# Kernel optimization log

Measured on AMD Instinct MI355X. Metric: run time of the kernel, lower is better.

The kernel has to match this reference:

```python
import jax, jax.numpy as jnp
import numpy as np

D_MODEL = 768
N_HEADS = 8
HEAD_DIM = D_MODEL // N_HEADS
LN_EPS = 1e-5

def setup_inputs() -> dict:
    key = jax.random.key(0)
    k1, k2, k3 = jax.random.split(key, 3)
    B, L = 8, 4096
    x = jax.random.normal(k1, (B, L, D_MODEL), dtype=jnp.float32)
    gamma = jnp.ones((D_MODEL,), dtype=jnp.float32)
    beta = jnp.zeros((D_MODEL,), dtype=jnp.float32)
    # torch Linear weights transposed so forward is x @ W
    w_qkv = jax.random.normal(k2, (D_MODEL, 3 * D_MODEL), dtype=jnp.float32) * (1.0 / np.sqrt(D_MODEL))
    w_out = jax.random.normal(k3, (D_MODEL, D_MODEL), dtype=jnp.float32) * (1.0 / np.sqrt(D_MODEL))
    return {"x": x, "gamma": gamma, "beta": beta, "w_qkv": w_qkv, "w_out": w_out}

def reference(x, gamma, beta, w_qkv, w_out):
    B, L, D = x.shape
    residual = x
    # LayerNorm
    mu = jnp.mean(x, axis=-1, keepdims=True)
    var = jnp.mean(jnp.square(x - mu), axis=-1, keepdims=True)
    xn = (x - mu) * jax.lax.rsqrt(var + LN_EPS) * gamma + beta
    # qkv projection, split, reshape to [B, H, L, d]
    qkv = xn @ w_qkv  # [B, L, 3D]
    q, k, v = jnp.split(qkv, 3, axis=-1)
    def to_heads(t):
        return t.reshape(B, L, N_HEADS, HEAD_DIM).transpose(0, 2, 1, 3)
    q, k, v = to_heads(q), to_heads(k), to_heads(v)
    # feature maps: elu + 1
    q = jax.nn.elu(q) + 1.0
    k = jax.nn.elu(k) + 1.0
    # linear attention: kv aggregation then query readout
    kv = jnp.einsum('bhld,bhlv->bhdv', k, v)          # [B,H,d,d]
    out = jnp.einsum('bhld,bhdv->bhlv', q, kv)         # [B,H,L,d]
    k_sum = jnp.sum(k, axis=2)                         # [B,H,d]
    normalizer = jnp.einsum('bhld,bhd->bhl', q, k_sum) # [B,H,L]
    normalizer = jnp.maximum(normalizer, 1e-6)
    out = out / normalizer[..., None]
    out = out.transpose(0, 2, 1, 3).reshape(B, L, D)
    out = out @ w_out
    return out + residual
```

## Files before the change

### kernel.cpp

```cpp
#include <hip/hip_runtime.h>
#include <stdint.h>

#define D_MODEL 768
#define N3      2304
#define NHEAD   8
#define DH      96
#define BATCH   8
#define SEQ     4096
#define ROWS    (BATCH*SEQ)
#define LN_EPS  1e-5f

typedef __attribute__((ext_vector_type(8))) __bf16 bf16x8;
typedef __attribute__((ext_vector_type(4))) float f32x4;
typedef __attribute__((ext_vector_type(8))) unsigned short ushort8;
typedef __attribute__((ext_vector_type(4))) unsigned short ushort4v;

__device__ __forceinline__ unsigned short f2bf(float f) {
  union { float f; unsigned int u; } v; v.f = f;
  unsigned int r = v.u + 0x7FFFu + ((v.u >> 16) & 1u);
  return (unsigned short)(r >> 16);
}
__device__ __forceinline__ float bf2f(unsigned short u) {
  union { unsigned int u; float f; } v; v.u = ((unsigned int)u) << 16;
  return v.f;
}

#define GLOBAL_LDS16(src, dst) \
  __builtin_amdgcn_global_load_lds((const __attribute__((address_space(1))) void*)(src), \
                                   (__attribute__((address_space(3))) void*)(dst), 16, 0, 0)

#define GATE(n) do { asm volatile("s_waitcnt vmcnt(" #n ")" ::: "memory"); \
                     __builtin_amdgcn_s_barrier(); asm volatile("" ::: "memory"); } while (0)

__global__ __launch_bounds__(256) void transpose_cast_kernel(
    const float* __restrict__ in, unsigned short* __restrict__ out, int R, int C) {
  __shared__ float tile[32][33];
  int c0 = blockIdx.x * 32, r0 = blockIdx.y * 32;
  int tx = threadIdx.x & 31, ty = threadIdx.x >> 5;
  #pragma unroll
  for (int i = ty; i < 32; i += 8)
    tile[i][tx] = in[(size_t)(r0 + i) * C + c0 + tx];
  __syncthreads();
  #pragma unroll
  for (int i = ty; i < 32; i += 8)
    out[(size_t)(c0 + i) * R + r0 + tx] = f2bf(tile[tx][i]);
}

__global__ __launch_bounds__(256) void ln_kernel(
    const float* __restrict__ x, const float* __restrict__ gamma,
    const float* __restrict__ beta, unsigned short* __restrict__ xn) {
  int wave = threadIdx.x >> 6, lane = threadIdx.x & 63;
  int row = blockIdx.x * 4 + wave;
  const float* xr = x + (size_t)row * D_MODEL;
  f32x4 v[3];
  float s = 0.f, sq = 0.f;
  #pragma unroll
  for (int i = 0; i < 3; ++i) {
    v[i] = *(const f32x4*)(xr + (i * 64 + lane) * 4);
    #pragma unroll
    for (int c = 0; c < 4; ++c) { s += v[i][c]; sq += v[i][c] * v[i][c]; }
  }
  #pragma unroll
  for (int o = 32; o; o >>= 1) {
    s  += __shfl_xor(s, o, 64);
    sq += __shfl_xor(sq, o, 64);
  }
  float mu  = s * (1.f / 768.f);
  float var = sq * (1.f / 768.f) - mu * mu;
  float rs  = rsqrtf(var + LN_EPS);
  #pragma unroll
  for (int i = 0; i < 3; ++i) {
    int col = (i * 64 + lane) * 4;
    ushort4v o;
    #pragma unroll
    for (int c = 0; c < 4; ++c)
      o[c] = f2bf((v[i][c] - mu) * rs * gamma[col + c] + beta[col + c]);
    *(ushort4v*)(xn + (size_t)row * D_MODEL + col) = o;
  }
}

__global__ __launch_bounds__(256, 3) void gemm_qkv128_kernel(
    const unsigned short* __restrict__ A, const unsigned short* __restrict__ Bt,
    unsigned short* __restrict__ qb, unsigned short* __restrict__ kT,
    unsigned short* __restrict__ vT) {
  __shared__ unsigned short As[3 * 4096];
  __shared__ unsigned short Bs[3 * 4096];
  const int K = D_MODEL, nbn = 18;
  int nwg = gridDim.x, id = blockIdx.x;
  int q8 = nwg >> 3;
  int wg = (id & 7) * q8 + (id >> 3);
  int bm = wg / nbn, bn = wg % nbn;

  const int lane = threadIdx.x & 63, wid = threadIdx.x >> 6;
  const int wm = wid >> 1, wn = wid & 1;
  const int l15 = lane & 15, hi = lane >> 4;
  const int colS = (hi ^ ((l15 >> 1) & 3)) << 3;
  const int srow = lane >> 2;
  const int scol = ((lane & 3) ^ ((lane >> 3) & 3)) << 3;

  const unsigned short* a0 = A  + (size_t)(bm * 128 +      wid * 16 + srow) * K + scol;
  const unsigned short* a1 = A  + (size_t)(bm * 128 + 64 + wid * 16 + srow) * K + scol;
  const unsigned short* b0 = Bt + (size_t)(bn * 128 +      wid * 16 + srow) * K + scol;
  const unsigned short* b1 = Bt + (size_t)(bn * 128 + 64 + wid * 16 + srow) * K + scol;
  auto stage = [&](int buf, int kt) {
    GLOBAL_LDS16(a0 + kt * 32, &As[buf * 4096 +        wid * 512]);
    GLOBAL_LDS16(a1 + kt * 32, &As[buf * 4096 + 2048 + wid * 512]);
    GLOBAL_LDS16(b0 + kt * 32, &Bs[buf * 4096 +        wid * 512]);
    GLOBAL_LDS16(b1 + kt * 32, &Bs[buf * 4096 + 2048 + wid * 512]);
  };

  f32x4 acc[4][4];
  #pragma unroll
  for (int i = 0; i < 4; ++i)
    #pragma unroll
    for (int j = 0; j < 4; ++j) acc[i][j] = (f32x4){0.f, 0.f, 0.f, 0.f};

#define QTILE(BUF, STG) do { \
    bf16x8 af[4], bv[4]; \
    _Pragma("unroll") for (int mf = 0; mf < 4; ++mf) \
      af[mf] = *(const bf16x8*)&As[(BUF) * 4096 + (wm * 64 + mf * 16 + l15) * 32 + colS]; \
    _Pragma("unroll") for (int nf = 0; nf < 4; ++nf) \
      bv[nf] = *(const bf16x8*)&Bs[(BUF) * 4096 + (wn * 64 + nf * 16 + l15) * 32 + colS]; \
    STG; \
    __builtin_amdgcn_s_setprio(1); \
    _Pragma("unroll") for (int mf = 0; mf < 4; ++mf) \
      _Pragma("unroll") for (int nf = 0; nf < 4; ++nf) \
        acc[mf][nf] = __builtin_amdgcn_mfma_f32_16x16x32_bf16( \
            af[mf], bv[nf], acc[mf][nf], 0, 0, 0); \
    __builtin_amdgcn_s_setprio(0); \
  } while (0)

  stage(0, 0); stage(1, 1);
  for (int it = 0; it < 7; ++it) {
    int T = 3 * it;
    GATE(4); QTILE(0, stage(2, T + 2));
    GATE(4); QTILE(1, stage(0, T + 3));
    GATE(4); QTILE(2, stage(1, T + 4));
  }
  GATE(4); QTILE(0, stage(2, 23));
  GATE(4); QTILE(1, {});
  GATE(0); QTILE(2, {});
#undef QTILE

  int r0 = bm * 128 + wm * 64, c0 = bn * 128 + wn * 64;
  if (bn < 6) {
    #pragma unroll
    for (int mf = 0; mf < 4; ++mf)
      #pragma unroll
      for (int nf = 0; nf < 4; ++nf) {
        int col = c0 + nf * 16 + l15;
        #pragma unroll
        for (int r = 0; r < 4; ++r) {
          int row = r0 + mf * 16 + hi * 4 + r;
          float v = acc[mf][nf][r];
          v = (v > 0.f) ? v + 1.f : __expf(v);
          qb[(size_t)row * D_MODEL + col] = f2bf(v);
        }
      }
  } else {
    const bool isK = (bn < 12);
    unsigned short* T = isK ? kT : vT;
    int cbase = c0 - (isK ? 768 : 1536);
    #pragma unroll
    for (int mf = 0; mf < 4; ++mf) {
      int lr = r0 + mf * 16 + hi * 4;
      int b = lr >> 12, lloc = lr & 4095;
      #pragma unroll
      for (int nf = 0; nf < 4; ++nf) {
        int cc = cbase + nf * 16 + l15;
        int h = cc / 96, d = cc - h * 96;
        ushort4v pk;
        #pragma unroll
        for (int r = 0; r < 4; ++r) {
          float v = acc[mf][nf][r];
          if (isK) v = (v > 0.f) ? v + 1.f : __expf(v);
          pk[r] = f2bf(v);
        }
        *(ushort4v*)&T[((size_t)(b * 8 + h) * 96 + d) * 4096 + lloc] = pk;
      }
    }
  }
}

__global__ __launch_bounds__(256, 3) void gemm_out_kernel(
    const unsigned short* __restrict__ A, const unsigned short* __restrict__ Bt,
    const float* __restrict__ resid, float* __restrict__ Cf) {
  __shared__ unsigned short As[3 * 4096];
  __shared__ unsigned short Bs[3 * 4096];
  const int K = D_MODEL, nbn = 6;
  int nwg = gridDim.x, id = blockIdx.x;
  int q8 = nwg >> 3;
  int wg = (id & 7) * q8 + (id >> 3);
  int bm = wg / nbn, bn = wg % nbn;

  const int lane = threadIdx.x & 63, wid = threadIdx.x >> 6;
  const int wm = wid >> 1, wn = wid & 1;
  const int l15 = lane & 15, hi = lane >> 4;
  const int colS = (hi ^ ((l15 >> 1) & 3)) << 3;
  const int srow = lane >> 2;
  const int scol = ((lane & 3) ^ ((lane >> 3) & 3)) << 3;

  const unsigned short* a0 = A  + (size_t)(bm * 128 +      wid * 16 + srow) * K + scol;
  const unsigned short* a1 = A  + (size_t)(bm * 128 + 64 + wid * 16 + srow) * K + scol;
  const unsigned short* b0 = Bt + (size_t)(bn * 128 +      wid * 16 + srow) * K + scol;
  const unsigned short* b1 = Bt + (size_t)(bn * 128 + 64 + wid * 16 + srow) * K + scol;
  auto stage = [&](int buf, int kt) {
    GLOBAL_LDS16(a0 + kt * 32, &As[buf * 4096 +        wid * 512]);
    GLOBAL_LDS16(a1 + kt * 32, &As[buf * 4096 + 2048 + wid * 512]);
    GLOBAL_LDS16(b0 + kt * 32, &Bs[buf * 4096 +        wid * 512]);
    GLOBAL_LDS16(b1 + kt * 32, &Bs[buf * 4096 + 2048 + wid * 512]);
  };

  f32x4 acc[4][4];
  #pragma unroll
  for (int i = 0; i < 4; ++i)
    #pragma unroll
    for (int j = 0; j < 4; ++j) acc[i][j] = (f32x4){0.f, 0.f, 0.f, 0.f};

#define HTILE(BUF, STG) do { \
    bf16x8 af[4], bv[4]; \
    _Pragma("unroll") for (int mf = 0; mf < 4; ++mf) \
      af[mf] = *(const bf16x8*)&As[(BUF) * 4096 + (wm * 64 + mf * 16 + l15) * 32 + colS]; \
    _Pragma("unroll") for (int nf = 0; nf < 4; ++nf) \
      bv[nf] = *(const bf16x8*)&Bs[(BUF) * 4096 + (wn * 64 + nf * 16 + l15) * 32 + colS]; \
    STG; \
    __builtin_amdgcn_s_setprio(1); \
    _Pragma("unroll") for (int mf = 0; mf < 4; ++mf) \
      _Pragma("unroll") for (int nf = 0; nf < 4; ++nf) \
        acc[mf][nf] = __builtin_amdgcn_mfma_f32_16x16x32_bf16( \
            af[mf], bv[nf], acc[mf][nf], 0, 0, 0); \
    __builtin_amdgcn_s_setprio(0); \
  } while (0)

  stage(0, 0); stage(1, 1);
  for (int it = 0; it < 7; ++it) {
    int T = 3 * it;
    GATE(4); HTILE(0, stage(2, T + 2));
    GATE(4); HTILE(1, stage(0, T + 3));
    GATE(4); HTILE(2, stage(1, T + 4));
  }
  GATE(4); HTILE(0, stage(2, 23));
  GATE(4); HTILE(1, {});
  GATE(0); HTILE(2, {});
#undef HTILE

  int r0 = bm * 128 + wm * 64, c0 = bn * 128 + wn * 64;
  #pragma unroll
  for (int mf = 0; mf < 4; ++mf)
    #pragma unroll
    for (int nf = 0; nf < 4; ++nf) {
      int col = c0 + nf * 16 + l15;
      #pragma unroll
      for (int r = 0; r < 4; ++r) {
        int row = r0 + mf * 16 + hi * 4 + r;
        Cf[(size_t)row * D_MODEL + col] =
            acc[mf][nf][r] + resid[(size_t)row * D_MODEL + col];
      }
    }
}

__global__ __launch_bounds__(256) void kvagg2_kernel(
    const unsigned short* __restrict__ kT, const unsigned short* __restrict__ vT,
    float* __restrict__ kvp) {
  __shared__ unsigned short KTs[3 * 6144];
  __shared__ unsigned short VTs[3 * 8192];
  int bh = blockIdx.x >> 2, chunk = blockIdx.x & 3;
  int tid = threadIdx.x;
  int lane = tid & 63, wid = tid >> 6;
  int l15 = lane & 15, hi = lane >> 4;

  #pragma unroll
  for (int i = 0; i < 3; ++i) {
    int s = i * 256 + tid;
    int buf = s >> 8, r = 96 + ((s >> 3) & 31), sl = s & 7;
    unsigned short val = (r == 96) ? (unsigned short)0x3F80 : (unsigned short)0;
    ushort8 v8 = {val, val, val, val, val, val, val, val};
    *(ushort8*)&VTs[buf * 8192 + r * 64 + sl * 8] = v8;
  }
  __syncthreads();

  const size_t kbase = ((size_t)bh * 96) * 4096 + chunk * 1024;
  auto stage = [&](int buf, int t) {
    #pragma unroll
    for (int i = 0; i < 3; ++i) {
      int sidx = i * 256 + tid;
      int row = sidx >> 3;
      int L = (sidx & 7) ^ (row & 7);
      size_t g = kbase + (size_t)row * 4096 + t * 64 + L * 8;
      GLOBAL_LDS16(kT + g, &KTs[buf * 6144 + (i * 256 + wid * 64) * 8]);
      GLOBAL_LDS16(vT + g, &VTs[buf * 8192 + (i * 256 + wid * 64) * 8]);
    }
  };

  f32x4 acc[6][2];
  #pragma unroll
  for (int i = 0; i < 6; ++i)
    #pragma unroll
    for (int j = 0; j < 2; ++j) acc[i][j] = (f32x4){0.f, 0.f, 0.f, 0.f};

#define KVTILE(BUF) do { \
    _Pragma("unroll") for (int kq = 0; kq < 2; ++kq) { \
      bf16x8 af[6], bv[2]; \
      _Pragma("unroll") for (int mf = 0; mf < 6; ++mf) { \
        int row = mf * 16 + l15; \
        af[mf] = *(const bf16x8*)&KTs[(BUF) * 6144 + row * 64 + ((kq * 4 + hi) ^ (row & 7)) * 8]; } \
      _Pragma("unroll") for (int nf = 0; nf < 2; ++nf) { \
        int row = wid * 32 + nf * 16 + l15; \
        bv[nf] = *(const bf16x8*)&VTs[(BUF) * 8192 + row * 64 + ((kq * 4 + hi) ^ (row & 7)) * 8]; } \
      __builtin_amdgcn_s_setprio(1); \
      _Pragma("unroll") for (int mf = 0; mf < 6; ++mf) \
        _Pragma("unroll") for (int nf = 0; nf < 2; ++nf) \
          acc[mf][nf] = __builtin_amdgcn_mfma_f32_16x16x32_bf16( \
              af[mf], bv[nf], acc[mf][nf], 0, 0, 0); \
      __builtin_amdgcn_s_setprio(0); \
    } } while (0)

  stage(0, 0); stage(1, 1);
  for (int t = 0; t < 14; ++t) {
    stage((t + 2) % 3, t + 2);
    GATE(12);
    KVTILE(t % 3);
  }
  GATE(6); KVTILE(2);
  GATE(0); KVTILE(0);
#undef KVTILE

  float* outp = kvp + ((size_t)bh * 4 + chunk) * (96 * 112);
  #pragma unroll
  for (int nf = 0; nf < 2; ++nf) {
    int e = wid * 32 + nf * 16 + l15;
    if (e < 112) {
      #pragma unroll
      for (int mf = 0; mf < 6; ++mf)
        #pragma unroll
        for (int r = 0; r < 4; ++r) {
          int d = mf * 16 + hi * 4 + r;
          outp[d * 112 + e] = acc[mf][nf][r];
        }
    }
  }
}

__global__ __launch_bounds__(256) void kvreduce_kernel(
    const float* __restrict__ kvp, unsigned short* __restrict__ kvTo) {
  int idx = blockIdx.x * 256 + threadIdx.x;
  if (idx >= 64 * 112 * 96) return;
  int d = idx % 96;
  int e = (idx / 96) % 112;
  int bh = idx / (96 * 112);
  float s = 0.f;
  #pragma unroll
  for (int c = 0; c < 4; ++c)
    s += kvp[(((size_t)bh * 4 + c) * 96 + d) * 112 + e];
  kvTo[idx] = f2bf(s);
}

__global__ __launch_bounds__(256) void readout_kernel(
    const unsigned short* __restrict__ qb, const unsigned short* __restrict__ kvT,
    unsigned short* __restrict__ attn) {
  __shared__ unsigned short Qs[128][104];
  __shared__ unsigned short Ks[112][104];
  int bh = blockIdx.x >> 5, lc = blockIdx.x & 31;
  int b = bh >> 3, h = bh & 7;
  int l0 = lc * 128;
  int wave = threadIdx.x >> 6, lane = threadIdx.x & 63;
  #pragma unroll
  for (int i = 0; i < 6; ++i) {
    int idx = i * 256 + threadIdx.x;
    int l = idx / 12, oc = idx % 12;
    size_t g = ((size_t)b * SEQ + l0 + l) * D_MODEL + h * DH + oc * 8;
    *(ushort8*)&Qs[l][oc * 8] = *(const ushort8*)(qb + g);
  }
  const unsigned short* kvbh = kvT + (size_t)bh * 112 * 96;
  #pragma unroll
  for (int i = 0; i < 6; ++i) {
    int idx = i * 256 + threadIdx.x;
    if (idx < 1344) {
      int e = idx / 12, oc = idx % 12;
      *(ushort8*)&Ks[e][oc * 8] = *(const ushort8*)(kvbh + e * 96 + oc * 8);
    }
  }
  __syncthreads();
  f32x4 acc[2][7];
  #pragma unroll
  for (int i = 0; i < 2; ++i)
    #pragma unroll
    for (int j = 0; j < 7; ++j) acc[i][j] = (f32x4){0.f, 0.f, 0.f, 0.f};
  #pragma unroll
  for (int kq = 0; kq < 3; ++kq) {
    int k0 = kq * 32 + (lane >> 4) * 8;
    bf16x8 af[2], bfv[7];
    #pragma unroll
    for (int i = 0; i < 2; ++i) af[i]  = *(const bf16x8*)&Qs[wave * 32 + i * 16 + (lane & 15)][k0];
    #pragma unroll
    for (int j = 0; j < 7; ++j) bfv[j] = *(const bf16x8*)&Ks[j * 16 + (lane & 15)][k0];
    #pragma unroll
    for (int i = 0; i < 2; ++i)
      #pragma unroll
      for (int j = 0; j < 7; ++j)
        acc[i][j] = __builtin_amdgcn_mfma_f32_16x16x32_bf16(af[i], bfv[j], acc[i][j], 0, 0, 0);
  }
  int g4 = lane >> 4;
  #pragma unroll
  for (int i = 0; i < 2; ++i) {
    #pragma unroll
    for (int r = 0; r < 4; ++r) {
      float nv = __shfl(acc[i][6][r], lane & 48, 64);
      float inv = 1.f / fmaxf(nv, 1e-6f);
      size_t orow = (size_t)b * SEQ + l0 + wave * 32 + i * 16 + g4 * 4 + r;
      #pragma unroll
      for (int j = 0; j < 6; ++j) {
        int col = h * DH + j * 16 + (lane & 15);
        attn[orow * D_MODEL + col] = f2bf(acc[i][j][r] * inv);
      }
    }
  }
}

extern "C" void kernel_launch(void* const* d_in, const int* in_sizes, int n_in,
                              void* d_out, int out_size, void* d_ws, size_t ws_size,
                              hipStream_t stream) {
  const float* x     = (const float*)d_in[0];
  const float* gamma = (const float*)d_in[1];
  const float* beta  = (const float*)d_in[2];
  const float* w_qkv = (const float*)d_in[3];
  const float* w_out = (const float*)d_in[4];
  float* out = (float*)d_out;

  char* ws = (char*)d_ws;
  size_t off = 0;
  auto alloc = [&](size_t bytes) -> void* {
    void* p = ws + off; off += (bytes + 255) & ~(size_t)255; return p;
  };
  unsigned short* xn    = (unsigned short*)alloc((size_t)ROWS * D_MODEL * 2);
  unsigned short* qb    = (unsigned short*)alloc((size_t)ROWS * D_MODEL * 2);
  unsigned short* kTb   = (unsigned short*)alloc((size_t)64 * 96 * SEQ * 2);
  unsigned short* vTb   = (unsigned short*)alloc((size_t)64 * 96 * SEQ * 2);
  unsigned short* wqkvT = (unsigned short*)alloc((size_t)N3 * D_MODEL * 2);
  unsigned short* woutT = (unsigned short*)alloc((size_t)D_MODEL * D_MODEL * 2);
  float* kvp            = (float*)alloc((size_t)256 * 96 * 112 * 4);
  unsigned short* kvT   = (unsigned short*)alloc((size_t)64 * 112 * 96 * 2);

  transpose_cast_kernel<<<dim3(N3 / 32, D_MODEL / 32), 256, 0, stream>>>(w_qkv, wqkvT, D_MODEL, N3);
  transpose_cast_kernel<<<dim3(D_MODEL / 32, D_MODEL / 32), 256, 0, stream>>>(w_out, woutT, D_MODEL, D_MODEL);
  ln_kernel<<<ROWS / 4, 256, 0, stream>>>(x, gamma, beta, xn);
  gemm_qkv128_kernel<<<(ROWS / 128) * (N3 / 128), 256, 0, stream>>>(xn, wqkvT, qb, kTb, vTb);
  kvagg2_kernel<<<256, 256, 0, stream>>>(kTb, vTb, kvp);
  kvreduce_kernel<<<(64 * 112 * 96 + 255) / 256, 256, 0, stream>>>(kvp, kvT);
  readout_kernel<<<2048, 256, 0, stream>>>(qb, kvT, xn);
  gemm_out_kernel<<<(ROWS / 128) * (D_MODEL / 128), 256, 0, stream>>>(xn, woutT, x, out);
}
```

Measured before the change: 336.3 us.

## Switch GEMMs to 32x32x16 MFMA and tile kT/vT layout by 128-row blocks

Both the QKV and output GEMMs now use 32x32x16 bf16 MFMA with 2x2 fragments per wave instead of 4x4 fragments of 16x16x32, so each wave issues fewer LDS fragment reads per k-step. The kT/vT intermediate is re-laid out as [bm][head][d][128] blocks so each QKV tile writes contiguous 128-element segments rather than strided rows of length 4096. The kv-aggregation loader is updated to index this blocked layout. The risk is epilogue stores with a different row/column mapping (16 rows per lane) and possibly higher register pressure.

```diff
diff --git a/kernel.cpp b/kernel.cpp
--- a/kernel.cpp
+++ b/kernel.cpp
@@ -12,6 +12,7 @@
 
 typedef __attribute__((ext_vector_type(8))) __bf16 bf16x8;
 typedef __attribute__((ext_vector_type(4))) float f32x4;
+typedef __attribute__((ext_vector_type(16))) float f32x16;
 typedef __attribute__((ext_vector_type(8))) unsigned short ushort8;
 typedef __attribute__((ext_vector_type(4))) unsigned short ushort4v;
 
@@ -93,8 +94,9 @@
 
   const int lane = threadIdx.x & 63, wid = threadIdx.x >> 6;
   const int wm = wid >> 1, wn = wid & 1;
-  const int l15 = lane & 15, hi = lane >> 4;
-  const int colS = (hi ^ ((l15 >> 1) & 3)) << 3;
+  const int l31 = lane & 31, l5 = lane >> 5;
+  const int sx0 = (l5 ^ ((lane >> 1) & 3)) << 3;
+  const int sx1 = ((2 + l5) ^ ((lane >> 1) & 3)) << 3;
   const int srow = lane >> 2;
   const int scol = ((lane & 3) ^ ((lane >> 3) & 3)) << 3;
 
@@ -109,24 +111,32 @@
     GLOBAL_LDS16(b1 + kt * 32, &Bs[buf * 4096 + 2048 + wid * 512]);
   };
 
-  f32x4 acc[4][4];
-  #pragma unroll
-  for (int i = 0; i < 4; ++i)
-    #pragma unroll
-    for (int j = 0; j < 4; ++j) acc[i][j] = (f32x4){0.f, 0.f, 0.f, 0.f};
+  f32x16 acc[2][2];
+  #pragma unroll
+  for (int i = 0; i < 2; ++i)
+    #pragma unroll
+    for (int j = 0; j < 2; ++j)
+      #pragma unroll
+      for (int r = 0; r < 16; ++r) acc[i][j][r] = 0.f;
 
 #define QTILE(BUF, STG) do { \
-    bf16x8 af[4], bv[4]; \
-    _Pragma("unroll") for (int mf = 0; mf < 4; ++mf) \
-      af[mf] = *(const bf16x8*)&As[(BUF) * 4096 + (wm * 64 + mf * 16 + l15) * 32 + colS]; \
-    _Pragma("unroll") for (int nf = 0; nf < 4; ++nf) \
-      bv[nf] = *(const bf16x8*)&Bs[(BUF) * 4096 + (wn * 64 + nf * 16 + l15) * 32 + colS]; \
+    bf16x8 af[2][2], bv[2][2]; \
+    _Pragma("unroll") for (int mf = 0; mf < 2; ++mf) { \
+      int rb = (BUF) * 4096 + (wm * 64 + mf * 32 + l31) * 32; \
+      af[mf][0] = *(const bf16x8*)&As[rb + sx0]; \
+      af[mf][1] = *(const bf16x8*)&As[rb + sx1]; } \
+    _Pragma("unroll") for (int nf = 0; nf < 2; ++nf) { \
+      int rb = (BUF) * 4096 + (wn * 64 + nf * 32 + l31) * 32; \
+      bv[nf][0] = *(const bf16x8*)&Bs[rb + sx0]; \
+      bv[nf][1] = *(const bf16x8*)&Bs[rb + sx1]; } \
     STG; \
     __builtin_amdgcn_s_setprio(1); \
-    _Pragma("unroll") for (int mf = 0; mf < 4; ++mf) \
-      _Pragma("unroll") for (int nf = 0; nf < 4; ++nf) \
-        acc[mf][nf] = __builtin_amdgcn_mfma_f32_16x16x32_bf16( \
-            af[mf], bv[nf], acc[mf][nf], 0, 0, 0); \
+    _Pragma("unroll") for (int mf = 0; mf < 2; ++mf) \
+      _Pragma("unroll") for (int nf = 0; nf < 2; ++nf) { \
+        acc[mf][nf] = __builtin_amdgcn_mfma_f32_32x32x16_bf16( \
+            af[mf][0], bv[nf][0], acc[mf][nf], 0, 0, 0); \
+        acc[mf][nf] = __builtin_amdgcn_mfma_f32_32x32x16_bf16( \
+            af[mf][1], bv[nf][1], acc[mf][nf], 0, 0, 0); } \
     __builtin_amdgcn_s_setprio(0); \
   } while (0)
 
@@ -145,13 +155,13 @@
   int r0 = bm * 128 + wm * 64, c0 = bn * 128 + wn * 64;
   if (bn < 6) {
     #pragma unroll
-    for (int mf = 0; mf < 4; ++mf)
-      #pragma unroll
-      for (int nf = 0; nf < 4; ++nf) {
-        int col = c0 + nf * 16 + l15;
+    for (int mf = 0; mf < 2; ++mf)
+      #pragma unroll
+      for (int nf = 0; nf < 2; ++nf) {
+        int col = c0 + nf * 32 + l31;
         #pragma unroll
-        for (int r = 0; r < 4; ++r) {
-          int row = r0 + mf * 16 + hi * 4 + r;
+        for (int r = 0; r < 16; ++r) {
+          int row = r0 + mf * 32 + (r & 3) + 8 * (r >> 2) + 4 * l5;
           float v = acc[mf][nf][r];
           v = (v > 0.f) ? v + 1.f : __expf(v);
           qb[(size_t)row * D_MODEL + col] = f2bf(v);
@@ -162,23 +172,25 @@
     unsigned short* T = isK ? kT : vT;
     int cbase = c0 - (isK ? 768 : 1536);
     #pragma unroll
-    for (int mf = 0; mf < 4; ++mf) {
-      int lr = r0 + mf * 16 + hi * 4;
-      int b = lr >> 12, lloc = lr & 4095;
-      #pragma unroll
-      for (int nf = 0; nf < 4; ++nf) {
-        int cc = cbase + nf * 16 + l15;
+    for (int mf = 0; mf < 2; ++mf)
+      #pragma unroll
+      for (int nf = 0; nf < 2; ++nf) {
+        int cc = cbase + nf * 32 + l31;
         int h = cc / 96, d = cc - h * 96;
-        ushort4v pk;
+        size_t rowb = (((size_t)bm * 8 + h) * 96 + d) * 128;
         #pragma unroll
-        for (int r = 0; r < 4; ++r) {
-          float v = acc[mf][nf][r];
-          if (isK) v = (v > 0.f) ? v + 1.f : __expf(v);
-          pk[r] = f2bf(v);
+        for (int rq = 0; rq < 4; ++rq) {
+          int ll = wm * 64 + mf * 32 + 8 * rq + 4 * l5;
+          ushort4v pk;
+          #pragma unroll
+          for (int j = 0; j < 4; ++j) {
+            float v = acc[mf][nf][rq * 4 + j];
+            if (isK) v = (v > 0.f) ? v + 1.f : __expf(v);
+            pk[j] = f2bf(v);
+          }
+          *(ushort4v*)&T[rowb + ll] = pk;
         }
-        *(ushort4v*)&T[((size_t)(b * 8 + h) * 96 + d) * 4096 + lloc] = pk;
       }
-    }
   }
 }
 
@@ -195,8 +207,9 @@
 
   const int lane = threadIdx.x & 63, wid = threadIdx.x >> 6;
   const int wm = wid >> 1, wn = wid & 1;
-  const int l15 = lane & 15, hi = lane >> 4;
-  const int colS = (hi ^ ((l15 >> 1) & 3)) << 3;
+  const int l31 = lane & 31, l5 = lane >> 5;
+  const int sx0 = (l5 ^ ((lane >> 1) & 3)) << 3;
+  const int sx1 = ((2 + l5) ^ ((lane >> 1) & 3)) << 3;
   const int srow = lane >> 2;
   const int scol = ((lane & 3) ^ ((lane >> 3) & 3)) << 3;
 
@@ -211,24 +224,32 @@
     GLOBAL_LDS16(b1 + kt * 32, &Bs[buf * 4096 + 2048 + wid * 512]);
   };
 
-  f32x4 acc[4][4];
-  #pragma unroll
-  for (int i = 0; i < 4; ++i)
-    #pragma unroll
-    for (int j = 0; j < 4; ++j) acc[i][j] = (f32x4){0.f, 0.f, 0.f, 0.f};
+  f32x16 acc[2][2];
+  #pragma unroll
+  for (int i = 0; i < 2; ++i)
+    #pragma unroll
+    for (int j = 0; j < 2; ++j)
+      #pragma unroll
+      for (int r = 0; r < 16; ++r) acc[i][j][r] = 0.f;
 
 #define HTILE(BUF, STG) do { \
-    bf16x8 af[4], bv[4]; \
-    _Pragma("unroll") for (int mf = 0; mf < 4; ++mf) \
-      af[mf] = *(const bf16x8*)&As[(BUF) * 4096 + (wm * 64 + mf * 16 + l15) * 32 + colS]; \
-    _Pragma("unroll") for (int nf = 0; nf < 4; ++nf) \
-      bv[nf] = *(const bf16x8*)&Bs[(BUF) * 4096 + (wn * 64 + nf * 16 + l15) * 32 + colS]; \
+    bf16x8 af[2][2], bv[2][2]; \
+    _Pragma("unroll") for (int mf = 0; mf < 2; ++mf) { \
+      int rb = (BUF) * 4096 + (wm * 64 + mf * 32 + l31) * 32; \
+      af[mf][0] = *(const bf16x8*)&As[rb + sx0]; \
+      af[mf][1] = *(const bf16x8*)&As[rb + sx1]; } \
+    _Pragma("unroll") for (int nf = 0; nf < 2; ++nf) { \
+      int rb = (BUF) * 4096 + (wn * 64 + nf * 32 + l31) * 32; \
+      bv[nf][0] = *(const bf16x8*)&Bs[rb + sx0]; \
+      bv[nf][1] = *(const bf16x8*)&Bs[rb + sx1]; } \
     STG; \
     __builtin_amdgcn_s_setprio(1); \
-    _Pragma("unroll") for (int mf = 0; mf < 4; ++mf) \
-      _Pragma("unroll") for (int nf = 0; nf < 4; ++nf) \
-        acc[mf][nf] = __builtin_amdgcn_mfma_f32_16x16x32_bf16( \
-            af[mf], bv[nf], acc[mf][nf], 0, 0, 0); \
+    _Pragma("unroll") for (int mf = 0; mf < 2; ++mf) \
+      _Pragma("unroll") for (int nf = 0; nf < 2; ++nf) { \
+        acc[mf][nf] = __builtin_amdgcn_mfma_f32_32x32x16_bf16( \
+            af[mf][0], bv[nf][0], acc[mf][nf], 0, 0, 0); \
+        acc[mf][nf] = __builtin_amdgcn_mfma_f32_32x32x16_bf16( \
+            af[mf][1], bv[nf][1], acc[mf][nf], 0, 0, 0); } \
     __builtin_amdgcn_s_setprio(0); \
   } while (0)
 
@@ -246,13 +267,13 @@
 
   int r0 = bm * 128 + wm * 64, c0 = bn * 128 + wn * 64;
   #pragma unroll
-  for (int mf = 0; mf < 4; ++mf)
-    #pragma unroll
-    for (int nf = 0; nf < 4; ++nf) {
-      int col = c0 + nf * 16 + l15;
-      #pragma unroll
-      for (int r = 0; r < 4; ++r) {
-        int row = r0 + mf * 16 + hi * 4 + r;
+  for (int mf = 0; mf < 2; ++mf)
+    #pragma unroll
+    for (int nf = 0; nf < 2; ++nf) {
+      int col = c0 + nf * 32 + l31;
+      #pragma unroll
+      for (int r = 0; r < 16; ++r) {
+        int row = r0 + mf * 32 + (r & 3) + 8 * (r >> 2) + 4 * l5;
         Cf[(size_t)row * D_MODEL + col] =
             acc[mf][nf][r] + resid[(size_t)row * D_MODEL + col];
       }
@@ -279,14 +300,15 @@
   }
   __syncthreads();
 
-  const size_t kbase = ((size_t)bh * 96) * 4096 + chunk * 1024;
+  const int b = bh >> 3, h = bh & 7;
   auto stage = [&](int buf, int t) {
     #pragma unroll
     for (int i = 0; i < 3; ++i) {
       int sidx = i * 256 + tid;
       int row = sidx >> 3;
       int L = (sidx & 7) ^ (row & 7);
-      size_t g = kbase + (size_t)row * 4096 + t * 64 + L * 8;
+      size_t g = ((((size_t)b * 32 + chunk * 8 + (t >> 1)) * 8 + h) * 96 + row) * 128
+               + (t & 1) * 64 + L * 8;
       GLOBAL_LDS16(kT + g, &KTs[buf * 6144 + (i * 256 + wid * 64) * 8]);
       GLOBAL_LDS16(vT + g, &VTs[buf * 8192 + (i * 256 + wid * 64) * 8]);
     }
```

After: 341.7 us. No clear change (+1.6%).

## Software-pipeline LDS fragment reads in QKV GEMM, tile K/V layout, fuse weight transposes

Applied to the files above, without the earlier changes.

The QKV GEMM main loop now double-buffers register fragments, so reads for the next K-tile from LDS overlap the MFMAs on the current one. It prefetches three stages up front and waits on lgkmcnt at each gate. The K/V transposed outputs are written in 128-token tiles per row block, and the kv-aggregation loader's addressing is changed to match, giving contiguous 256-byte segments. The two weight transpose launches are merged into a single kernel. Holding extra fragment registers may lower occupancy below the launch-bounds target.

```diff
diff --git a/kernel.cpp b/kernel.cpp
--- a/kernel.cpp
+++ b/kernel.cpp
@@ -31,11 +31,18 @@
 
 #define GATE(n) do { asm volatile("s_waitcnt vmcnt(" #n ")" ::: "memory"); \
                      __builtin_amdgcn_s_barrier(); asm volatile("" ::: "memory"); } while (0)
-
-__global__ __launch_bounds__(256) void transpose_cast_kernel(
-    const float* __restrict__ in, unsigned short* __restrict__ out, int R, int C) {
+#define GATEP(n) do { asm volatile("s_waitcnt vmcnt(" #n ") lgkmcnt(0)" ::: "memory"); \
+                      __builtin_amdgcn_s_barrier(); asm volatile("" ::: "memory"); } while (0)
+
+__global__ __launch_bounds__(256) void transpose2_kernel(
+    const float* __restrict__ wqkv, const float* __restrict__ wout,
+    unsigned short* __restrict__ wqkvT, unsigned short* __restrict__ woutT) {
   __shared__ float tile[32][33];
-  int c0 = blockIdx.x * 32, r0 = blockIdx.y * 32;
+  int bx = blockIdx.x;
+  const float* in; unsigned short* out; int C, c0;
+  if (bx < 72) { in = wqkv; out = wqkvT; C = N3;      c0 = bx * 32; }
+  else         { in = wout; out = woutT; C = D_MODEL; c0 = (bx - 72) * 32; }
+  int r0 = blockIdx.y * 32;
   int tx = threadIdx.x & 31, ty = threadIdx.x >> 5;
   #pragma unroll
   for (int i = ty; i < 32; i += 8)
@@ -43,7 +50,7 @@
   __syncthreads();
   #pragma unroll
   for (int i = ty; i < 32; i += 8)
-    out[(size_t)(c0 + i) * R + r0 + tx] = f2bf(tile[tx][i]);
+    out[(size_t)(c0 + i) * D_MODEL + r0 + tx] = f2bf(tile[tx][i]);
 }
 
 __global__ __launch_bounds__(256) void ln_kernel(
@@ -79,13 +86,13 @@
   }
 }
 
-__global__ __launch_bounds__(256, 3) void gemm_qkv128_kernel(
+__global__ __launch_bounds__(256, 3) void gemm_qkv_p_kernel(
     const unsigned short* __restrict__ A, const unsigned short* __restrict__ Bt,
     unsigned short* __restrict__ qb, unsigned short* __restrict__ kT,
     unsigned short* __restrict__ vT) {
   __shared__ unsigned short As[3 * 4096];
   __shared__ unsigned short Bs[3 * 4096];
-  const int K = D_MODEL, nbn = 18;
+  const int K = D_MODEL, nbn = 18, NKT = 24;
   int nwg = gridDim.x, id = blockIdx.x;
   int q8 = nwg >> 3;
   int wg = (id & 7) * q8 + (id >> 3);
@@ -115,32 +122,44 @@
     #pragma unroll
     for (int j = 0; j < 4; ++j) acc[i][j] = (f32x4){0.f, 0.f, 0.f, 0.f};
 
-#define QTILE(BUF, STG) do { \
-    bf16x8 af[4], bv[4]; \
+  bf16x8 afA[4], bvA[4], afB[4], bvB[4];
+
+#define READF(BUF, AF, BV) do { int _o = (BUF) * 4096; \
     _Pragma("unroll") for (int mf = 0; mf < 4; ++mf) \
-      af[mf] = *(const bf16x8*)&As[(BUF) * 4096 + (wm * 64 + mf * 16 + l15) * 32 + colS]; \
+      AF[mf] = *(const bf16x8*)&As[_o + (wm * 64 + mf * 16 + l15) * 32 + colS]; \
     _Pragma("unroll") for (int nf = 0; nf < 4; ++nf) \
-      bv[nf] = *(const bf16x8*)&Bs[(BUF) * 4096 + (wn * 64 + nf * 16 + l15) * 32 + colS]; \
-    STG; \
-    __builtin_amdgcn_s_setprio(1); \
+      BV[nf] = *(const bf16x8*)&Bs[_o + (wn * 64 + nf * 16 + l15) * 32 + colS]; \
+  } while (0)
+#define MMX(AF, BV) do { __builtin_amdgcn_s_setprio(1); \
     _Pragma("unroll") for (int mf = 0; mf < 4; ++mf) \
       _Pragma("unroll") for (int nf = 0; nf < 4; ++nf) \
         acc[mf][nf] = __builtin_amdgcn_mfma_f32_16x16x32_bf16( \
-            af[mf], bv[nf], acc[mf][nf], 0, 0, 0); \
+            AF[mf], BV[nf], acc[mf][nf], 0, 0, 0); \
     __builtin_amdgcn_s_setprio(0); \
   } while (0)
 
-  stage(0, 0); stage(1, 1);
-  for (int it = 0; it < 7; ++it) {
-    int T = 3 * it;
-    GATE(4); QTILE(0, stage(2, T + 2));
-    GATE(4); QTILE(1, stage(0, T + 3));
-    GATE(4); QTILE(2, stage(1, T + 4));
-  }
-  GATE(4); QTILE(0, stage(2, 23));
-  GATE(4); QTILE(1, {});
-  GATE(0); QTILE(2, {});
-#undef QTILE
+  stage(0, 0); stage(1, 1); stage(2, 2);
+  GATEP(8);
+  READF(0, afA, bvA);
+
+  #pragma unroll
+  for (int i = 0; i < 11; ++i) {
+    int t = 2 * i;
+    GATEP(4);
+    stage(t % 3, t + 3);
+    READF((t + 1) % 3, afB, bvB);
+    MMX(afA, bvA);
+    GATEP(4);
+    if (i < 10) stage((t + 1) % 3, t + 4);
+    READF((t + 2) % 3, afA, bvA);
+    MMX(afB, bvB);
+  }
+  GATEP(0);
+  READF(2, afB, bvB);
+  MMX(afA, bvA);
+  MMX(afB, bvB);
+#undef READF
+#undef MMX
 
   int r0 = bm * 128 + wm * 64, c0 = bn * 128 + wn * 64;
   if (bn < 6) {
@@ -163,8 +182,7 @@
     int cbase = c0 - (isK ? 768 : 1536);
     #pragma unroll
     for (int mf = 0; mf < 4; ++mf) {
-      int lr = r0 + mf * 16 + hi * 4;
-      int b = lr >> 12, lloc = lr & 4095;
+      int ll = wm * 64 + mf * 16 + hi * 4;
       #pragma unroll
       for (int nf = 0; nf < 4; ++nf) {
         int cc = cbase + nf * 16 + l15;
@@ -176,7 +194,7 @@
           if (isK) v = (v > 0.f) ? v + 1.f : __expf(v);
           pk[r] = f2bf(v);
         }
-        *(ushort4v*)&T[((size_t)(b * 8 + h) * 96 + d) * 4096 + lloc] = pk;
+        *(ushort4v*)&T[(((size_t)bm * 8 + h) * 96 + d) * 128 + ll] = pk;
       }
     }
   }
@@ -279,14 +297,15 @@
   }
   __syncthreads();
 
-  const size_t kbase = ((size_t)bh * 96) * 4096 + chunk * 1024;
+  const int b = bh >> 3, h = bh & 7;
   auto stage = [&](int buf, int t) {
     #pragma unroll
     for (int i = 0; i < 3; ++i) {
       int sidx = i * 256 + tid;
       int row = sidx >> 3;
       int L = (sidx & 7) ^ (row & 7);
-      size_t g = kbase + (size_t)row * 4096 + t * 64 + L * 8;
+      size_t g = ((((size_t)b * 32 + chunk * 8 + (t >> 1)) * 8 + h) * 96 + row) * 128
+               + (t & 1) * 64 + L * 8;
       GLOBAL_LDS16(kT + g, &KTs[buf * 6144 + (i * 256 + wid * 64) * 8]);
       GLOBAL_LDS16(vT + g, &VTs[buf * 8192 + (i * 256 + wid * 64) * 8]);
     }
@@ -441,10 +460,9 @@
   float* kvp            = (float*)alloc((size_t)256 * 96 * 112 * 4);
   unsigned short* kvT   = (unsigned short*)alloc((size_t)64 * 112 * 96 * 2);
 
-  transpose_cast_kernel<<<dim3(N3 / 32, D_MODEL / 32), 256, 0, stream>>>(w_qkv, wqkvT, D_MODEL, N3);
-  transpose_cast_kernel<<<dim3(D_MODEL / 32, D_MODEL / 32), 256, 0, stream>>>(w_out, woutT, D_MODEL, D_MODEL);
+  transpose2_kernel<<<dim3(96, 24), 256, 0, stream>>>(w_qkv, w_out, wqkvT, woutT);
   ln_kernel<<<ROWS / 4, 256, 0, stream>>>(x, gamma, beta, xn);
-  gemm_qkv128_kernel<<<(ROWS / 128) * (N3 / 128), 256, 0, stream>>>(xn, wqkvT, qb, kTb, vTb);
+  gemm_qkv_p_kernel<<<(ROWS / 128) * (N3 / 128), 256, 0, stream>>>(xn, wqkvT, qb, kTb, vTb);
   kvagg2_kernel<<<256, 256, 0, stream>>>(kTb, vTb, kvp);
   kvreduce_kernel<<<(64 * 112 * 96 + 255) / 256, 256, 0, stream>>>(kvp, kvT);
   readout_kernel<<<2048, 256, 0, stream>>>(qb, kvT, xn);
```

Measured after the change: 327.9 us. 2.5% less time.

## Widen QKV GEMM tile to 128x256 and store K/V in blocked layout

Applied to the files above, without the earlier changes.

The QKV projection GEMM now uses 128x256 tiles, with each wave owning all 128 rows and a 64-column slice. This raises MFMA work per LDS A-fragment load and halves the number of workgroups, at the cost of more accumulator registers and lower occupancy (2 waves per SIMD). K and V are written in a per-128-row blocked transposed layout so each tile writes contiguous 256-byte runs, and the kv aggregation kernel's loads are remapped to match. The two weight transpose launches are merged into one kernel to save a launch.

```diff
diff --git a/kernel.cpp b/kernel.cpp
--- a/kernel.cpp
+++ b/kernel.cpp
@@ -32,10 +32,15 @@
 #define GATE(n) do { asm volatile("s_waitcnt vmcnt(" #n ")" ::: "memory"); \
                      __builtin_amdgcn_s_barrier(); asm volatile("" ::: "memory"); } while (0)
 
-__global__ __launch_bounds__(256) void transpose_cast_kernel(
-    const float* __restrict__ in, unsigned short* __restrict__ out, int R, int C) {
+__global__ __launch_bounds__(256) void transpose2_kernel(
+    const float* __restrict__ wqkv, const float* __restrict__ wout,
+    unsigned short* __restrict__ wqkvT, unsigned short* __restrict__ woutT) {
   __shared__ float tile[32][33];
-  int c0 = blockIdx.x * 32, r0 = blockIdx.y * 32;
+  int bx = blockIdx.x;
+  const float* in; unsigned short* out; int C, c0;
+  if (bx < 72) { in = wqkv; out = wqkvT; C = N3;      c0 = bx * 32; }
+  else         { in = wout; out = woutT; C = D_MODEL; c0 = (bx - 72) * 32; }
+  int r0 = blockIdx.y * 32;
   int tx = threadIdx.x & 31, ty = threadIdx.x >> 5;
   #pragma unroll
   for (int i = ty; i < 32; i += 8)
@@ -43,7 +48,7 @@
   __syncthreads();
   #pragma unroll
   for (int i = ty; i < 32; i += 8)
-    out[(size_t)(c0 + i) * R + r0 + tx] = f2bf(tile[tx][i]);
+    out[(size_t)(c0 + i) * D_MODEL + r0 + tx] = f2bf(tile[tx][i]);
 }
 
 __global__ __launch_bounds__(256) void ln_kernel(
@@ -79,20 +84,20 @@
   }
 }
 
-__global__ __launch_bounds__(256, 3) void gemm_qkv128_kernel(
+__global__ __launch_bounds__(256, 2) void gemm_qkv_w_kernel(
     const unsigned short* __restrict__ A, const unsigned short* __restrict__ Bt,
     unsigned short* __restrict__ qb, unsigned short* __restrict__ kT,
     unsigned short* __restrict__ vT) {
   __shared__ unsigned short As[3 * 4096];
-  __shared__ unsigned short Bs[3 * 4096];
-  const int K = D_MODEL, nbn = 18;
+  __shared__ unsigned short Bs[3 * 8192];
+  const int K = D_MODEL, nbn = 9;
   int nwg = gridDim.x, id = blockIdx.x;
   int q8 = nwg >> 3;
   int wg = (id & 7) * q8 + (id >> 3);
   int bm = wg / nbn, bn = wg % nbn;
 
   const int lane = threadIdx.x & 63, wid = threadIdx.x >> 6;
-  const int wm = wid >> 1, wn = wid & 1;
+  const int wn = wid;
   const int l15 = lane & 15, hi = lane >> 4;
   const int colS = (hi ^ ((l15 >> 1) & 3)) << 3;
   const int srow = lane >> 2;
@@ -100,30 +105,34 @@
 
   const unsigned short* a0 = A  + (size_t)(bm * 128 +      wid * 16 + srow) * K + scol;
   const unsigned short* a1 = A  + (size_t)(bm * 128 + 64 + wid * 16 + srow) * K + scol;
-  const unsigned short* b0 = Bt + (size_t)(bn * 128 +      wid * 16 + srow) * K + scol;
-  const unsigned short* b1 = Bt + (size_t)(bn * 128 + 64 + wid * 16 + srow) * K + scol;
+  const unsigned short* b0 = Bt + (size_t)(bn * 256 + wid * 64 +      srow) * K + scol;
+  const unsigned short* b1 = Bt + (size_t)(bn * 256 + wid * 64 + 16 + srow) * K + scol;
+  const unsigned short* b2 = Bt + (size_t)(bn * 256 + wid * 64 + 32 + srow) * K + scol;
+  const unsigned short* b3 = Bt + (size_t)(bn * 256 + wid * 64 + 48 + srow) * K + scol;
   auto stage = [&](int buf, int kt) {
     GLOBAL_LDS16(a0 + kt * 32, &As[buf * 4096 +        wid * 512]);
     GLOBAL_LDS16(a1 + kt * 32, &As[buf * 4096 + 2048 + wid * 512]);
-    GLOBAL_LDS16(b0 + kt * 32, &Bs[buf * 4096 +        wid * 512]);
-    GLOBAL_LDS16(b1 + kt * 32, &Bs[buf * 4096 + 2048 + wid * 512]);
+    GLOBAL_LDS16(b0 + kt * 32, &Bs[buf * 8192 + wid * 2048]);
+    GLOBAL_LDS16(b1 + kt * 32, &Bs[buf * 8192 + wid * 2048 + 512]);
+    GLOBAL_LDS16(b2 + kt * 32, &Bs[buf * 8192 + wid * 2048 + 1024]);
+    GLOBAL_LDS16(b3 + kt * 32, &Bs[buf * 8192 + wid * 2048 + 1536]);
   };
 
-  f32x4 acc[4][4];
-  #pragma unroll
-  for (int i = 0; i < 4; ++i)
+  f32x4 acc[8][4];
+  #pragma unroll
+  for (int i = 0; i < 8; ++i)
     #pragma unroll
     for (int j = 0; j < 4; ++j) acc[i][j] = (f32x4){0.f, 0.f, 0.f, 0.f};
 
 #define QTILE(BUF, STG) do { \
-    bf16x8 af[4], bv[4]; \
-    _Pragma("unroll") for (int mf = 0; mf < 4; ++mf) \
-      af[mf] = *(const bf16x8*)&As[(BUF) * 4096 + (wm * 64 + mf * 16 + l15) * 32 + colS]; \
+    bf16x8 af[8], bv[4]; \
+    _Pragma("unroll") for (int mf = 0; mf < 8; ++mf) \
+      af[mf] = *(const bf16x8*)&As[(BUF) * 4096 + (mf * 16 + l15) * 32 + colS]; \
     _Pragma("unroll") for (int nf = 0; nf < 4; ++nf) \
-      bv[nf] = *(const bf16x8*)&Bs[(BUF) * 4096 + (wn * 64 + nf * 16 + l15) * 32 + colS]; \
+      bv[nf] = *(const bf16x8*)&Bs[(BUF) * 8192 + (wn * 64 + nf * 16 + l15) * 32 + colS]; \
     STG; \
     __builtin_amdgcn_s_setprio(1); \
-    _Pragma("unroll") for (int mf = 0; mf < 4; ++mf) \
+    _Pragma("unroll") for (int mf = 0; mf < 8; ++mf) \
       _Pragma("unroll") for (int nf = 0; nf < 4; ++nf) \
         acc[mf][nf] = __builtin_amdgcn_mfma_f32_16x16x32_bf16( \
             af[mf], bv[nf], acc[mf][nf], 0, 0, 0); \
@@ -133,19 +142,19 @@
   stage(0, 0); stage(1, 1);
   for (int it = 0; it < 7; ++it) {
     int T = 3 * it;
-    GATE(4); QTILE(0, stage(2, T + 2));
-    GATE(4); QTILE(1, stage(0, T + 3));
-    GATE(4); QTILE(2, stage(1, T + 4));
-  }
-  GATE(4); QTILE(0, stage(2, 23));
-  GATE(4); QTILE(1, {});
+    GATE(6); QTILE(0, stage(2, T + 2));
+    GATE(6); QTILE(1, stage(0, T + 3));
+    GATE(6); QTILE(2, stage(1, T + 4));
+  }
+  GATE(6); QTILE(0, stage(2, 23));
+  GATE(6); QTILE(1, {});
   GATE(0); QTILE(2, {});
 #undef QTILE
 
-  int r0 = bm * 128 + wm * 64, c0 = bn * 128 + wn * 64;
-  if (bn < 6) {
-    #pragma unroll
-    for (int mf = 0; mf < 4; ++mf)
+  int r0 = bm * 128, c0 = bn * 256 + wn * 64;
+  if (bn < 3) {
+    #pragma unroll
+    for (int mf = 0; mf < 8; ++mf)
       #pragma unroll
       for (int nf = 0; nf < 4; ++nf) {
         int col = c0 + nf * 16 + l15;
@@ -158,13 +167,12 @@
         }
       }
   } else {
-    const bool isK = (bn < 12);
+    const bool isK = (bn < 6);
     unsigned short* T = isK ? kT : vT;
     int cbase = c0 - (isK ? 768 : 1536);
     #pragma unroll
-    for (int mf = 0; mf < 4; ++mf) {
-      int lr = r0 + mf * 16 + hi * 4;
-      int b = lr >> 12, lloc = lr & 4095;
+    for (int mf = 0; mf < 8; ++mf) {
+      int ll = mf * 16 + hi * 4;
       #pragma unroll
       for (int nf = 0; nf < 4; ++nf) {
         int cc = cbase + nf * 16 + l15;
@@ -176,7 +184,7 @@
           if (isK) v = (v > 0.f) ? v + 1.f : __expf(v);
           pk[r] = f2bf(v);
         }
-        *(ushort4v*)&T[((size_t)(b * 8 + h) * 96 + d) * 4096 + lloc] = pk;
+        *(ushort4v*)&T[(((size_t)bm * 8 + h) * 96 + d) * 128 + ll] = pk;
       }
     }
   }
@@ -279,14 +287,15 @@
   }
   __syncthreads();
 
-  const size_t kbase = ((size_t)bh * 96) * 4096 + chunk * 1024;
+  const int b = bh >> 3, h = bh & 7;
   auto stage = [&](int buf, int t) {
     #pragma unroll
     for (int i = 0; i < 3; ++i) {
       int sidx = i * 256 + tid;
       int row = sidx >> 3;
       int L = (sidx & 7) ^ (row & 7);
-      size_t g = kbase + (size_t)row * 4096 + t * 64 + L * 8;
+      size_t g = ((((size_t)b * 32 + chunk * 8 + (t >> 1)) * 8 + h) * 96 + row) * 128
+               + (t & 1) * 64 + L * 8;
       GLOBAL_LDS16(kT + g, &KTs[buf * 6144 + (i * 256 + wid * 64) * 8]);
       GLOBAL_LDS16(vT + g, &VTs[buf * 8192 + (i * 256 + wid * 64) * 8]);
     }
@@ -441,10 +450,9 @@
   float* kvp            = (float*)alloc((size_t)256 * 96 * 112 * 4);
   unsigned short* kvT   = (unsigned short*)alloc((size_t)64 * 112 * 96 * 2);
 
-  transpose_cast_kernel<<<dim3(N3 / 32, D_MODEL / 32), 256, 0, stream>>>(w_qkv, wqkvT, D_MODEL, N3);
-  transpose_cast_kernel<<<dim3(D_MODEL / 32, D_MODEL / 32), 256, 0, stream>>>(w_out, woutT, D_MODEL, D_MODEL);
+  transpose2_kernel<<<dim3(96, 24), 256, 0, stream>>>(w_qkv, w_out, wqkvT, woutT);
   ln_kernel<<<ROWS / 4, 256, 0, stream>>>(x, gamma, beta, xn);
-  gemm_qkv128_kernel<<<(ROWS / 128) * (N3 / 128), 256, 0, stream>>>(xn, wqkvT, qb, kTb, vTb);
+  gemm_qkv_w_kernel<<<(ROWS / 128) * (N3 / 256), 256, 0, stream>>>(xn, wqkvT, qb, kTb, vTb);
   kvagg2_kernel<<<256, 256, 0, stream>>>(kTb, vTb, kvp);
   kvreduce_kernel<<<(64 * 112 * 96 + 255) / 256, 256, 0, stream>>>(kvp, kvT);
   readout_kernel<<<2048, 256, 0, stream>>>(qb, kvT, xn);
```

Measured after the change: 326.0 us. 1.03x faster.
